# Kernel tuning notes

Hardware: AMD Instinct MI355X
Metric: run time of the kernel (lower is better)

## Reference

```python
import jax, jax.numpy as jnp
import numpy as np

H, W, CIN, COUT, B = 56, 56, 64, 64, 32
K = 3            # kernel_size
WIN = 15         # win_range
R = (WIN - 1) // 2


def _make_sample_idx():
    """Per-pixel fixed random sample locations within a WINxWIN window,
    mirroring Dconv_drop.__init__ (random.sample over valid window indices)."""
    rng = np.random.default_rng(0)
    ii = np.arange(H)[:, None, None]          # [H,1,1]
    jj = np.arange(W)[None, :, None]          # [1,W,1]
    lo_i = np.maximum(0, ii - R); hi_i = np.minimum(H - 1, ii + R)
    lo_j = np.maximum(0, jj - R); hi_j = np.minimum(W - 1, jj + R)
    ri = rng.integers(np.broadcast_to(lo_i, (H, W, K * K)),
                      np.broadcast_to(hi_i, (H, W, K * K)) + 1)
    rj = rng.integers(np.broadcast_to(lo_j, (H, W, K * K)),
                      np.broadcast_to(hi_j, (H, W, K * K)) + 1)
    return (ri * W + rj).astype(np.int32)    # [H,W,9] indices into H*W


def setup_inputs() -> dict:
    key = jax.random.key(0)
    k1, k2 = jax.random.split(key)
    x = jax.random.normal(k1, (B, CIN, H, W), dtype=jnp.float32)
    weight = jax.random.normal(k2, (COUT, CIN, K, K), dtype=jnp.float32) * 0.05
    sample_idx = jnp.asarray(_make_sample_idx())
    return {"x": x, "weight": weight, "sample_idx": sample_idx}


def reference(x, weight, sample_idx):
    # x: [B,C,H,W]; sample_idx: [H,W,9] flat indices into H*W.
    # Original: scatter gathered pixels into [B,C,3H,3W] grid, then
    # stride-3 kernel-3 conv => per-pixel contraction over the 9 samples.
    b, c, h, w = x.shape
    x_flat = x.reshape(b, c, h * w)
    gathered = x_flat[:, :, sample_idx]              # [B,C,H,W,9]
    w_flat = weight.reshape(weight.shape[0], c, K * K)  # [O,C,9]
    out = jnp.einsum('bchwk,ock->bohw', gathered, w_flat)
    return out
```

## Files before the change

kernel.cpp:

```cpp
#include <hip/hip_runtime.h>
#include <hip/hip_bf16.h>

#define HH 56
#define WW 56
#define CIN 64
#define COUT 64
#define BATCH 32
#define KK 9
#define HWP (HH*WW)
#define NS 18
#define NTILE 49
#define NBLK (NTILE*BATCH)
#define XT_OFF 73728
#define XSW 33

typedef __attribute__((ext_vector_type(8))) short short8;
typedef __attribute__((ext_vector_type(4))) float float4v;
typedef __attribute__((ext_vector_type(4))) unsigned int uint4v;

__device__ __forceinline__ unsigned short f2bf(float f) {
    union { float f; unsigned u; } v; v.f = f;
    unsigned r = v.u + 0x7FFFu + ((v.u >> 16) & 1u);
    return (unsigned short)(r >> 16);
}

__device__ __forceinline__ void prepack_elem(const float* __restrict__ w,
                                             unsigned short* __restrict__ apack,
                                             int e) {
    int j = e & 7;
    int l = (e >> 3) & 63;
    int ss = e >> 9;
    int mb = ss / 18;
    int s  = ss - mb * 18;
    int o = mb * 16 + (l & 15);
    int c = ((s & 1) << 5) + ((l >> 4) << 3) + j;
    int k = s >> 1;
    apack[e] = f2bf(w[(o * CIN + c) * KK + k]);
}

__global__ __launch_bounds__(256) void prep_kernel(
    const float* __restrict__ x, const float* __restrict__ w,
    unsigned int* __restrict__ xt, unsigned short* __restrict__ apack)
{
    int bid = blockIdx.x;
    int t   = threadIdx.x;
    if (bid < 3136) {
        int u   = bid * 256 + t;
        int c2q = u & 7;
        int hwb = u >> 3;
        int b   = hwb / HWP;
        int hw  = hwb - b * HWP;
        const float* xb = x + ((size_t)b * CIN + c2q * 8) * HWP + hw;
        uint4v o;
        #pragma unroll
        for (int i = 0; i < 4; ++i) {
            float f0 = xb[(size_t)(2 * i) * HWP];
            float f1 = xb[(size_t)(2 * i + 1) * HWP];
            o[i] = (unsigned)f2bf(f0) | ((unsigned)f2bf(f1) << 16);
        }
        *(uint4v*)(xt + (size_t)hwb * 32 + c2q * 4) = o;
    } else {
        prepack_elem(w, apack, (bid - 3136) * 256 + t);
    }
}

__global__ __launch_bounds__(256) void prep_weights_only(
    const float* __restrict__ w, unsigned short* __restrict__ apack)
{
    prepack_elem(w, apack, blockIdx.x * 256 + threadIdx.x);
}

__global__ __launch_bounds__(256) void dconv_main(
    const unsigned int* __restrict__ xt, const int* __restrict__ sidx,
    const unsigned short* __restrict__ apack, float* __restrict__ out)
{
    __shared__ unsigned int xs[496 * 16];

    const int t    = threadIdx.x;
    const int lane = t & 63;
    const int wv   = t >> 6;
    const int mbp  = wv >> 1;
    const int ntp  = wv & 1;
    const int col  = lane & 15;
    const int krow = lane >> 4;

    int bid  = blockIdx.x;
    int orig = (bid & 7) * 196 + (bid >> 3);
    int b    = orig / NTILE;
    int bx   = orig - b * NTILE;
    int ti = bx / 7, tj = bx - (bx / 7) * 7;
    int r0 = ti * 8 - 7; if (r0 < 0) r0 = 0;
    int c0 = tj * 8 - 7; if (c0 < 0) c0 = 0;

    const unsigned int* xtb = xt + (size_t)b * HWP * 32;


    int lb[2][KK];
    #pragma unroll
    for (int nn = 0; nn < 2; ++nn) {
        int p  = (ntp * 2 + nn) * 16 + col;
        int gi = ti * 8 + (p >> 3), gj = tj * 8 + (p & 7);
        const int* sp = sidx + (gi * WW + gj) * KK;
        #pragma unroll
        for (int k = 0; k < KK; ++k) {
            int g  = sp[k];
            int si = g / WW, sj = g - si * WW;
            int row = (si - r0) * 22 + (sj - c0);
            lb[nn][k] = row * 64 + ((krow ^ (row & 3)) << 4);
        }
    }

    const unsigned short* apW = apack + (size_t)(mbp * 2 * NS) * 512 + lane * 8;

    float4v zero = {0.f, 0.f, 0.f, 0.f};
    float4v acc[2][2] = {{zero, zero}, {zero, zero}};
    const char* xsb = (const char*)xs;

    #pragma unroll
    for (int sh = 0; sh < 2; ++sh) {
        for (int grp = wv; grp < 31; grp += 4) {
            int row = grp * 16 + (lane >> 2);
            int rc  = row < 483 ? row : 483;
            int lsr = rc / 22;
            int lsc = rc - lsr * 22;
            int si = r0 + lsr; if (si > HH - 1) si = HH - 1;
            int sj = c0 + lsc; if (sj > WW - 1) sj = WW - 1;
            int q  = (lane & 3) ^ (rc & 3);
            const unsigned int* src =
                xtb + (size_t)(si * WW + sj) * 32 + sh * 16 + (q << 2);
            __builtin_amdgcn_global_load_lds(
                (const __attribute__((address_space(1))) unsigned int*)src,
                (__attribute__((address_space(3))) unsigned int*)(xs + grp * 256),
                16, 0, 0);
        }
        __syncthreads();

        #pragma unroll
        for (int k = 0; k < KK; ++k) {
            short8 a0 = *(const short8*)(apW + (size_t)(2 * k + sh) * 512);
            short8 a1 = *(const short8*)(apW + (size_t)(NS + 2 * k + sh) * 512);
            #pragma unroll
            for (int nn = 0; nn < 2; ++nn) {
                short8 bv = *(const short8*)(xsb + lb[nn][k]);
                acc[0][nn] = __builtin_amdgcn_mfma_f32_16x16x32_bf16(
                    a0, bv, acc[0][nn], 0, 0, 0);
                acc[1][nn] = __builtin_amdgcn_mfma_f32_16x16x32_bf16(
                    a1, bv, acc[1][nn], 0, 0, 0);
            }
        }
        __syncthreads();
    }

    float* ob = out + ((size_t)b * COUT + mbp * 32) * HWP;
    #pragma unroll
    for (int m = 0; m < 2; ++m) {
        #pragma unroll
        for (int nn = 0; nn < 2; ++nn) {
            int p = (ntp * 2 + nn) * 16 + col;
            int g = (ti * 8 + (p >> 3)) * WW + tj * 8 + (p & 7);
            #pragma unroll
            for (int r = 0; r < 4; ++r)
                ob[(m * 16 + krow * 4 + r) * HWP + g] = acc[m][nn][r];
        }
    }
}

__global__ __launch_bounds__(256, 2) void dconv_fb(
    const float* __restrict__ x, const int* __restrict__ sidx,
    const unsigned short* __restrict__ apack, float* __restrict__ out)
{
    __shared__ unsigned int xs[484 * XSW];

    const int t    = threadIdx.x;
    const int lane = t & 63;
    const int wv   = t >> 6;
    const int mbp  = wv >> 1;
    const int ntp  = wv & 1;
    const int col  = lane & 15;
    const int krow = lane >> 4;
    const int bx   = blockIdx.x;
    const int b    = blockIdx.y;
    const int ti = bx / 7, tj = bx - (bx / 7) * 7;
    int r0 = ti * 8 - 7; if (r0 < 0) r0 = 0;
    int r1 = ti * 8 + 14; if (r1 > HH - 1) r1 = HH - 1;
    int c0 = tj * 8 - 7; if (c0 < 0) c0 = 0;
    int c1 = tj * 8 + 14; if (c1 > WW - 1) c1 = WW - 1;

    int lb[2][KK];
    #pragma unroll
    for (int nn = 0; nn < 2; ++nn) {
        int p  = (ntp * 2 + nn) * 16 + col;
        int gi = ti * 8 + (p >> 3), gj = tj * 8 + (p & 7);
        const int* sp = sidx + (gi * WW + gj) * KK;
        #pragma unroll
        for (int k = 0; k < KK; ++k) {
            int g  = sp[k];
            int si = g / WW, sj = g - si * WW;
            lb[nn][k] = ((si - r0) * 22 + (sj - c0)) * (XSW * 4);
        }
    }

    short8 areg[2][NS];
    #pragma unroll
    for (int m = 0; m < 2; ++m) {
        const unsigned short* ap = apack + ((mbp * 2 + m) * NS) * 512 + lane * 8;
        #pragma unroll
        for (int s = 0; s < NS; ++s)
            areg[m][s] = *(const short8*)(ap + s * 512);
    }

    const float* xb = x + (size_t)b * CIN * HWP;
    for (int e = t; e < 32 * 512; e += 256) {
        int c2 = e >> 9, ls = e & 511;
        if (ls < 484) {
            int lsr = ls / 22;
            int si = r0 + lsr, sj = c0 + (ls - lsr * 22);
            if (si <= r1 && sj <= c1) {
                int g = si * WW + sj;
                float f0 = xb[(2 * c2) * HWP + g];
                float f1 = xb[(2 * c2 + 1) * HWP + g];
                xs[ls * XSW + c2] =
                    (unsigned)f2bf(f0) | ((unsigned)f2bf(f1) << 16);
            }
        }
    }
    __syncthreads();

    float4v zero = {0.f, 0.f, 0.f, 0.f};
    float4v acc[2][2] = {{zero, zero}, {zero, zero}};
    const char* xsb = (const char*)xs + krow * 16;

    #pragma unroll
    for (int k = 0; k < KK; ++k) {
        #pragma unroll
        for (int nn = 0; nn < 2; ++nn) {
            const char* ba = xsb + lb[nn][k];
            union { int i[4]; short8 s8; } b0, b1;
            #pragma unroll
            for (int w = 0; w < 4; ++w) {
                b0.i[w] = *(const int*)(ba + w * 4);
                b1.i[w] = *(const int*)(ba + 64 + w * 4);
            }
            acc[0][nn] = __builtin_amdgcn_mfma_f32_16x16x32_bf16(
                areg[0][2 * k], b0.s8, acc[0][nn], 0, 0, 0);
            acc[1][nn] = __builtin_amdgcn_mfma_f32_16x16x32_bf16(
                areg[1][2 * k], b0.s8, acc[1][nn], 0, 0, 0);
            acc[0][nn] = __builtin_amdgcn_mfma_f32_16x16x32_bf16(
                areg[0][2 * k + 1], b1.s8, acc[0][nn], 0, 0, 0);
            acc[1][nn] = __builtin_amdgcn_mfma_f32_16x16x32_bf16(
                areg[1][2 * k + 1], b1.s8, acc[1][nn], 0, 0, 0);
        }
    }

    float* ob = out + ((size_t)b * COUT + mbp * 32) * HWP;
    #pragma unroll
    for (int m = 0; m < 2; ++m) {
        #pragma unroll
        for (int nn = 0; nn < 2; ++nn) {
            int p = (ntp * 2 + nn) * 16 + col;
            int g = (ti * 8 + (p >> 3)) * WW + tj * 8 + (p & 7);
            #pragma unroll
            for (int r = 0; r < 4; ++r)
                ob[(m * 16 + krow * 4 + r) * HWP + g] = acc[m][nn][r];
        }
    }
}

extern "C" void kernel_launch(void* const* d_in, const int* in_sizes, int n_in,
                              void* d_out, int out_size, void* d_ws, size_t ws_size,
                              hipStream_t stream) {
    const float* x    = (const float*)d_in[0];
    const float* w    = (const float*)d_in[1];
    const int*   sidx = (const int*)d_in[2];
    float* out = (float*)d_out;
    unsigned short* apack = (unsigned short*)d_ws;
    unsigned int*   xt    = (unsigned int*)((char*)d_ws + XT_OFF);

    size_t need = (size_t)XT_OFF + (size_t)BATCH * HWP * 128;
    if (ws_size >= need) {
        prep_kernel<<<3280, 256, 0, stream>>>(x, w, xt, apack);
        dconv_main<<<NBLK, 256, 0, stream>>>(xt, sidx, apack, out);
    } else {
        prep_weights_only<<<144, 256, 0, stream>>>(w, apack);
        dim3 grid(NTILE, BATCH);
        dconv_fb<<<grid, 256, 0, stream>>>(x, sidx, apack, out);
    }
}
```

Measured before the change: 33.94 us.

## Switch main conv to 32x32x16 MFMA with LDS-staged weights and vectorized prep

Reworks the main kernel so that each wave runs a single 32x32x16 bf16 MFMA per tap instead of four 16x16x32 MFMAs. Channels are processed in four 16-channel chunks with a smaller LDS input tile, and the weight fragments are staged into LDS through global_load_lds. The prep kernel now reads float4 vectors along the spatial dimension and writes four pixels per thread, and the weight packing layout is changed to match the new MFMA fragments. This aims to cut MFMA issue count, improve prep-kernel memory coalescing and raise occupancy (launch bounds set to 4 blocks per CU). In exchange it adds twice as many barrier phases and drops the LDS bank swizzle, which risks bank conflicts.

```diff
diff --git a/kernel.cpp b/kernel.cpp
--- a/kernel.cpp
+++ b/kernel.cpp
@@ -8,14 +8,15 @@
 #define BATCH 32
 #define KK 9
 #define HWP (HH*WW)
-#define NS 18
 #define NTILE 49
 #define NBLK (NTILE*BATCH)
 #define XT_OFF 73728
 #define XSW 33
+#define NS 18
 
 typedef __attribute__((ext_vector_type(8))) short short8;
 typedef __attribute__((ext_vector_type(4))) float float4v;
+typedef __attribute__((ext_vector_type(16))) float f32x16;
 typedef __attribute__((ext_vector_type(4))) unsigned int uint4v;
 
 __device__ __forceinline__ unsigned short f2bf(float f) {
@@ -24,9 +25,53 @@
     return (unsigned short)(r >> 16);
 }
 
-__device__ __forceinline__ void prepack_elem(const float* __restrict__ w,
-                                             unsigned short* __restrict__ apack,
-                                             int e) {
+__global__ __launch_bounds__(256) void prep_kernel(
+    const float* __restrict__ x, const float* __restrict__ w,
+    unsigned int* __restrict__ xt, unsigned short* __restrict__ apack)
+{
+    int bid = blockIdx.x;
+    int t   = threadIdx.x;
+    if (bid < 784) {
+        int u   = bid * 256 + t;
+        int c2q = u & 7;
+        int hq  = u >> 3;
+        int b   = hq / 784;
+        int q   = hq - b * 784;
+        int hw  = q * 4;
+        const float* xb = x + ((size_t)b * CIN + c2q * 8) * HWP + hw;
+        float4v f[8];
+        #pragma unroll
+        for (int i = 0; i < 8; ++i)
+            f[i] = *(const float4v*)(xb + (size_t)i * HWP);
+        unsigned int* xto = xt + ((size_t)b * HWP + hw) * 32 + c2q * 4;
+        #pragma unroll
+        for (int j = 0; j < 4; ++j) {
+            uint4v o;
+            #pragma unroll
+            for (int ci = 0; ci < 4; ++ci)
+                o[ci] = (unsigned)f2bf(f[2 * ci][j]) |
+                        ((unsigned)f2bf(f[2 * ci + 1][j]) << 16);
+            *(uint4v*)(xto + (size_t)j * 32) = o;
+        }
+    } else {
+        int e = (bid - 784) * 256 + t;
+        int j = e & 7;
+        int l = (e >> 3) & 63;
+        int line = e >> 9;
+        int mbb = line / 36;
+        int s   = line - mbb * 36;
+        int p   = s & 3;
+        int tap = s >> 2;
+        int o = mbb * 32 + (l & 31);
+        int c = p * 16 + ((l >> 5) << 3) + j;
+        apack[e] = f2bf(w[(o * CIN + c) * KK + tap]);
+    }
+}
+
+__global__ __launch_bounds__(256) void prep_weights_only(
+    const float* __restrict__ w, unsigned short* __restrict__ apack)
+{
+    int e = blockIdx.x * 256 + threadIdx.x;
     int j = e & 7;
     int l = (e >> 3) & 63;
     int ss = e >> 9;
@@ -38,51 +83,18 @@
     apack[e] = f2bf(w[(o * CIN + c) * KK + k]);
 }
 
-__global__ __launch_bounds__(256) void prep_kernel(
-    const float* __restrict__ x, const float* __restrict__ w,
-    unsigned int* __restrict__ xt, unsigned short* __restrict__ apack)
-{
-    int bid = blockIdx.x;
-    int t   = threadIdx.x;
-    if (bid < 3136) {
-        int u   = bid * 256 + t;
-        int c2q = u & 7;
-        int hwb = u >> 3;
-        int b   = hwb / HWP;
-        int hw  = hwb - b * HWP;
-        const float* xb = x + ((size_t)b * CIN + c2q * 8) * HWP + hw;
-        uint4v o;
-        #pragma unroll
-        for (int i = 0; i < 4; ++i) {
-            float f0 = xb[(size_t)(2 * i) * HWP];
-            float f1 = xb[(size_t)(2 * i + 1) * HWP];
-            o[i] = (unsigned)f2bf(f0) | ((unsigned)f2bf(f1) << 16);
-        }
-        *(uint4v*)(xt + (size_t)hwb * 32 + c2q * 4) = o;
-    } else {
-        prepack_elem(w, apack, (bid - 3136) * 256 + t);
-    }
-}
-
-__global__ __launch_bounds__(256) void prep_weights_only(
-    const float* __restrict__ w, unsigned short* __restrict__ apack)
-{
-    prepack_elem(w, apack, blockIdx.x * 256 + threadIdx.x);
-}
-
-__global__ __launch_bounds__(256) void dconv_main(
+__global__ __launch_bounds__(256, 4) void dconv_main(
     const unsigned int* __restrict__ xt, const int* __restrict__ sidx,
     const unsigned short* __restrict__ apack, float* __restrict__ out)
 {
-    __shared__ unsigned int xs[496 * 16];
+    __shared__ unsigned int xs[496 * 8];
+    __shared__ unsigned int aLds[18 * 256];
 
     const int t    = threadIdx.x;
     const int lane = t & 63;
     const int wv   = t >> 6;
-    const int mbp  = wv >> 1;
-    const int ntp  = wv & 1;
-    const int col  = lane & 15;
-    const int krow = lane >> 4;
+    const int mbb  = wv >> 1;
+    const int ntb  = wv & 1;
 
     int bid  = blockIdx.x;
     int orig = (bid & 7) * 196 + (bid >> 3);
@@ -94,74 +106,62 @@
 
     const unsigned int* xtb = xt + (size_t)b * HWP * 32;
 
-
-    int lb[2][KK];
-    #pragma unroll
-    for (int nn = 0; nn < 2; ++nn) {
-        int p  = (ntp * 2 + nn) * 16 + col;
-        int gi = ti * 8 + (p >> 3), gj = tj * 8 + (p & 7);
-        const int* sp = sidx + (gi * WW + gj) * KK;
-        #pragma unroll
-        for (int k = 0; k < KK; ++k) {
-            int g  = sp[k];
-            int si = g / WW, sj = g - si * WW;
-            int row = (si - r0) * 22 + (sj - c0);
-            lb[nn][k] = row * 64 + ((krow ^ (row & 3)) << 4);
-        }
-    }
-
-    const unsigned short* apW = apack + (size_t)(mbp * 2 * NS) * 512 + lane * 8;
-
-    float4v zero = {0.f, 0.f, 0.f, 0.f};
-    float4v acc[2][2] = {{zero, zero}, {zero, zero}};
-    const char* xsb = (const char*)xs;
-
-    #pragma unroll
-    for (int sh = 0; sh < 2; ++sh) {
-        for (int grp = wv; grp < 31; grp += 4) {
-            int row = grp * 16 + (lane >> 2);
-            int rc  = row < 483 ? row : 483;
-            int lsr = rc / 22;
-            int lsc = rc - lsr * 22;
+    int pt = ntb * 32 + (lane & 31);
+    int gi = ti * 8 + (pt >> 3), gj = tj * 8 + (pt & 7);
+    const int* sp = sidx + (gi * WW + gj) * KK;
+    int lb[KK];
+    #pragma unroll
+    for (int k = 0; k < KK; ++k) {
+        int g  = sp[k];
+        int si = g / WW, sj = g - si * WW;
+        lb[k] = ((si - r0) * 22 + (sj - c0)) * 32 + ((lane >> 5) << 4);
+    }
+
+    f32x16 acc;
+    #pragma unroll
+    for (int r = 0; r < 16; ++r) acc[r] = 0.f;
+
+    for (int p = 0; p < 4; ++p) {
+        for (int grp = wv; grp < 16; grp += 4) {
+            int rr = grp * 32 + (lane >> 1);
+            int rc = rr < 483 ? rr : 483;
+            int lsr = rc / 22, lsc = rc - lsr * 22;
             int si = r0 + lsr; if (si > HH - 1) si = HH - 1;
             int sj = c0 + lsc; if (sj > WW - 1) sj = WW - 1;
-            int q  = (lane & 3) ^ (rc & 3);
             const unsigned int* src =
-                xtb + (size_t)(si * WW + sj) * 32 + sh * 16 + (q << 2);
+                xtb + (size_t)(si * WW + sj) * 32 + p * 8 + ((lane & 1) << 2);
             __builtin_amdgcn_global_load_lds(
                 (const __attribute__((address_space(1))) unsigned int*)src,
                 (__attribute__((address_space(3))) unsigned int*)(xs + grp * 256),
                 16, 0, 0);
         }
+        for (int grp = wv; grp < 18; grp += 4) {
+            int mb2 = grp / 9, tap = grp - mb2 * 9;
+            const unsigned short* srcA =
+                apack + (size_t)(mb2 * 36 + tap * 4 + p) * 512 + lane * 8;
+            __builtin_amdgcn_global_load_lds(
+                (const __attribute__((address_space(1))) unsigned int*)srcA,
+                (__attribute__((address_space(3))) unsigned int*)(aLds + grp * 256),
+                16, 0, 0);
+        }
         __syncthreads();
 
         #pragma unroll
-        for (int k = 0; k < KK; ++k) {
-            short8 a0 = *(const short8*)(apW + (size_t)(2 * k + sh) * 512);
-            short8 a1 = *(const short8*)(apW + (size_t)(NS + 2 * k + sh) * 512);
-            #pragma unroll
-            for (int nn = 0; nn < 2; ++nn) {
-                short8 bv = *(const short8*)(xsb + lb[nn][k]);
-                acc[0][nn] = __builtin_amdgcn_mfma_f32_16x16x32_bf16(
-                    a0, bv, acc[0][nn], 0, 0, 0);
-                acc[1][nn] = __builtin_amdgcn_mfma_f32_16x16x32_bf16(
-                    a1, bv, acc[1][nn], 0, 0, 0);
-            }
+        for (int tap = 0; tap < KK; ++tap) {
+            short8 aF = *(const short8*)((const char*)aLds +
+                                         (mbb * 9 + tap) * 1024 + lane * 16);
+            short8 bF = *(const short8*)((const char*)xs + lb[tap]);
+            acc = __builtin_amdgcn_mfma_f32_32x32x16_bf16(aF, bF, acc, 0, 0, 0);
         }
         __syncthreads();
     }
 
-    float* ob = out + ((size_t)b * COUT + mbp * 32) * HWP;
-    #pragma unroll
-    for (int m = 0; m < 2; ++m) {
-        #pragma unroll
-        for (int nn = 0; nn < 2; ++nn) {
-            int p = (ntp * 2 + nn) * 16 + col;
-            int g = (ti * 8 + (p >> 3)) * WW + tj * 8 + (p & 7);
-            #pragma unroll
-            for (int r = 0; r < 4; ++r)
-                ob[(m * 16 + krow * 4 + r) * HWP + g] = acc[m][nn][r];
-        }
+    float* ob = out + ((size_t)b * COUT + mbb * 32) * HWP;
+    int g = gi * WW + gj;
+    #pragma unroll
+    for (int r = 0; r < 16; ++r) {
+        int oloc = (r & 3) + ((r >> 2) << 3) + ((lane >> 5) << 2);
+        ob[(size_t)oloc * HWP + g] = acc[r];
     }
 }
 
@@ -278,7 +278,7 @@
 
     size_t need = (size_t)XT_OFF + (size_t)BATCH * HWP * 128;
     if (ws_size >= need) {
-        prep_kernel<<<3280, 256, 0, stream>>>(x, w, xt, apack);
+        prep_kernel<<<928, 256, 0, stream>>>(x, w, xt, apack);
         dconv_main<<<NBLK, 256, 0, stream>>>(xt, sidx, apack, out);
     } else {
         prep_weights_only<<<144, 256, 0, stream>>>(w, apack);
```

Result: slower. 37.24 us (+9.7%).

## Vectorize x transpose prep and prefetch weight fragments before barrier

Applied to the files above, without the earlier changes.

The prep kernel now has each thread load four consecutive pixels per channel as float4 vectors and write four packed bf16 rows, replacing scalar loads with one pixel per thread. This cuts the prep grid from 3280 to 928 blocks and widens global reads. In the main kernel, all 18 weight fragments per stage are loaded into registers before the barrier, so their global latency overlaps the async LDS fill rather than sitting inside the MFMA loop. A launch bound of 3 blocks per SM is added, which caps register use and risks spills given the larger register footprint.

```diff
diff --git a/kernel.cpp b/kernel.cpp
--- a/kernel.cpp
+++ b/kernel.cpp
@@ -44,23 +44,30 @@
 {
     int bid = blockIdx.x;
     int t   = threadIdx.x;
-    if (bid < 3136) {
+    if (bid < 784) {
         int u   = bid * 256 + t;
         int c2q = u & 7;
-        int hwb = u >> 3;
-        int b   = hwb / HWP;
-        int hw  = hwb - b * HWP;
+        int hq  = u >> 3;
+        int b   = hq / 784;
+        int q   = hq - b * 784;
+        int hw  = q * 4;
         const float* xb = x + ((size_t)b * CIN + c2q * 8) * HWP + hw;
-        uint4v o;
-        #pragma unroll
-        for (int i = 0; i < 4; ++i) {
-            float f0 = xb[(size_t)(2 * i) * HWP];
-            float f1 = xb[(size_t)(2 * i + 1) * HWP];
-            o[i] = (unsigned)f2bf(f0) | ((unsigned)f2bf(f1) << 16);
-        }
-        *(uint4v*)(xt + (size_t)hwb * 32 + c2q * 4) = o;
+        float4v f[8];
+        #pragma unroll
+        for (int i = 0; i < 8; ++i)
+            f[i] = *(const float4v*)(xb + (size_t)i * HWP);
+        unsigned int* xto = xt + ((size_t)b * HWP + hw) * 32 + c2q * 4;
+        #pragma unroll
+        for (int j = 0; j < 4; ++j) {
+            uint4v o;
+            #pragma unroll
+            for (int ci = 0; ci < 4; ++ci)
+                o[ci] = (unsigned)f2bf(f[2 * ci][j]) |
+                        ((unsigned)f2bf(f[2 * ci + 1][j]) << 16);
+            *(uint4v*)(xto + (size_t)j * 32) = o;
+        }
     } else {
-        prepack_elem(w, apack, (bid - 3136) * 256 + t);
+        prepack_elem(w, apack, (bid - 784) * 256 + t);
     }
 }
 
@@ -70,7 +77,7 @@
     prepack_elem(w, apack, blockIdx.x * 256 + threadIdx.x);
 }
 
-__global__ __launch_bounds__(256) void dconv_main(
+__global__ __launch_bounds__(256, 3) void dconv_main(
     const unsigned int* __restrict__ xt, const int* __restrict__ sidx,
     const unsigned short* __restrict__ apack, float* __restrict__ out)
 {
@@ -93,7 +100,6 @@
     int c0 = tj * 8 - 7; if (c0 < 0) c0 = 0;
 
     const unsigned int* xtb = xt + (size_t)b * HWP * 32;
-
 
     int lb[2][KK];
     #pragma unroll
@@ -133,19 +139,26 @@
                 (__attribute__((address_space(3))) unsigned int*)(xs + grp * 256),
                 16, 0, 0);
         }
+
+        short8 aR[2][KK];
+        #pragma unroll
+        for (int m = 0; m < 2; ++m)
+            #pragma unroll
+            for (int k = 0; k < KK; ++k)
+                aR[m][k] = *(const short8*)(apW +
+                            (size_t)(m * NS + 2 * k + sh) * 512);
+
         __syncthreads();
 
         #pragma unroll
         for (int k = 0; k < KK; ++k) {
-            short8 a0 = *(const short8*)(apW + (size_t)(2 * k + sh) * 512);
-            short8 a1 = *(const short8*)(apW + (size_t)(NS + 2 * k + sh) * 512);
             #pragma unroll
             for (int nn = 0; nn < 2; ++nn) {
                 short8 bv = *(const short8*)(xsb + lb[nn][k]);
                 acc[0][nn] = __builtin_amdgcn_mfma_f32_16x16x32_bf16(
-                    a0, bv, acc[0][nn], 0, 0, 0);
+                    aR[0][k], bv, acc[0][nn], 0, 0, 0);
                 acc[1][nn] = __builtin_amdgcn_mfma_f32_16x16x32_bf16(
-                    a1, bv, acc[1][nn], 0, 0, 0);
+                    aR[1][k], bv, acc[1][nn], 0, 0, 0);
             }
         }
         __syncthreads();
@@ -278,7 +291,7 @@
 
     size_t need = (size_t)XT_OFF + (size_t)BATCH * HWP * 128;
     if (ws_size >= need) {
-        prep_kernel<<<3280, 256, 0, stream>>>(x, w, xt, apack);
+        prep_kernel<<<928, 256, 0, stream>>>(x, w, xt, apack);
         dconv_main<<<NBLK, 256, 0, stream>>>(xt, sidx, apack, out);
     } else {
         prep_weights_only<<<144, 256, 0, stream>>>(w, apack);
```

Measured after the change: 35.58 us. 4.8% more time.
